# Kernel tuning notes

Hardware: AMD Instinct MI355X
Metric: run time of the kernel (lower is better)

Reference implementation:

```python
import jax, jax.numpy as jnp
import numpy as np
import math

N_ROW, N_COL, MID_DIM = 16, 16, 256
B, S, D, K, N_NEURONS = 4, 4096, 1024, 8, 64


def setup_inputs() -> dict:
    key = jax.random.key(0)
    ks = jax.random.split(key, 8)
    return {
        "x": jax.random.normal(ks[0], (B, S, D), dtype=jnp.float32),
        "neuron_idx": jax.random.randint(ks[1], (B, S, K), 0, N_NEURONS),
        "neuron_weights": jax.random.uniform(ks[2], (B, S, K), dtype=jnp.float32),
        "neuron_recipe": jax.random.normal(ks[3], (N_NEURONS, N_ROW * N_COL), dtype=jnp.float32) * 0.02,
        "row_basis": jax.random.normal(ks[4], (N_ROW, D, MID_DIM), dtype=jnp.float32) * 0.02,
        "col_basis": jax.random.normal(ks[5], (N_COL, MID_DIM, D), dtype=jnp.float32) * 0.02,
        "out_w": jax.random.normal(ks[6], (D, D), dtype=jnp.float32) * 0.02,
        "out_b": jnp.zeros((D,), dtype=jnp.float32),
        "alpha": jnp.asarray(0.1, dtype=jnp.float32),
    }


def reference(x, neuron_idx, neuron_weights, neuron_recipe, row_basis, col_basis, out_w, out_b, alpha):
    Bx, Sx, Dx = x.shape
    # --- recipe routing: gather per-token recipes, softmax, weighted sum ---
    sel = neuron_recipe[neuron_idx]                     # [B,S,k,RC]
    sel = jax.nn.softmax(sel, axis=-1)
    token_recipe = jnp.sum(sel * neuron_weights[..., None], axis=2)  # [B,S,RC]
    recipe = jax.nn.softmax(token_recipe, axis=-1).reshape(Bx, Sx, N_ROW, N_COL)
    row_w = recipe.sum(axis=-1)                         # [B,S,n_row]
    col_w = recipe.sum(axis=-2)                         # [B,S,n_col]
    # --- dynamic Q/K: sum over basis middle/last axis commutes with contraction ---
    q = jnp.einsum('bsr,rm->bsm', row_w, row_basis.sum(axis=1))  # [B,S,mid]
    kk = jnp.einsum('bsc,cm->bsm', col_w, col_basis.sum(axis=2)) # [B,S,mid]
    scores = jnp.einsum('bsm,btm->bst', q, kk) / math.sqrt(MID_DIM)  # [B,S,S]
    causal = jnp.triu(jnp.ones((Sx, Sx), dtype=bool), k=1)
    scores = jnp.where(causal, -jnp.inf, scores)
    attn = jax.nn.softmax(scores, axis=-1)
    context = jnp.einsum('bst,btd->bsd', attn, x)        # [B,S,D]
    transform = jnp.einsum('bsc,cd->bsd', col_w, col_basis.sum(axis=1))  # [B,S,D]
    out = jax.nn.gelu(context + alpha * transform, approximate=False)
    return out @ out_w.T + out_b
```

## Files before the change

### kernel.cpp

```cpp
#include <hip/hip_runtime.h>
#include <hip/hip_bf16.h>
#include <math.h>

#define BB 4
#define SS 4096
#define DDIM 1024
#define KSEL 8
#define NR 16
#define NC 16
#define MID 256
#define RC 256
#define TOK (BB*SS)

typedef __hip_bfloat16 bf16;
typedef short short8 __attribute__((ext_vector_type(8)));
typedef short short4v __attribute__((ext_vector_type(4)));
typedef float floatx4 __attribute__((ext_vector_type(4)));
typedef float floatx16 __attribute__((ext_vector_type(16)));
#define MFMA16(a,b,c) __builtin_amdgcn_mfma_f32_16x16x32_bf16(a,b,c,0,0,0)
#define MFMA32(a,b,c) __builtin_amdgcn_mfma_f32_32x32x16_bf16(a,b,c,0,0,0)

__device__ __forceinline__ float uihf(unsigned v) { union { unsigned i; float f; } t; t.i = v; return t.f; }
__device__ __forceinline__ float b2f(bf16 h) { return __bfloat162float(h); }
__device__ __forceinline__ float bs2f(short s) { return uihf(((unsigned)(unsigned short)s) << 16); }
__device__ __forceinline__ short f2bs(float f) {
    bf16 h = __float2bfloat16(f);
    return *reinterpret_cast<short*>(&h);
}
__device__ __forceinline__ float loadf(const void* p, size_t i, bool f32m) {
    return f32m ? ((const float*)p)[i] : b2f(((const bf16*)p)[i]);
}

#define WS_RB   16
#define WS_CB2  4112
#define WS_CB1  8208
#define WS_CW   24592
#define WS_BIAS 286736
#define WS_QK   287760
#define WS_WB   4482064
#define WS_XT   5006352
#define WS_LV   13394960

struct DetectArgs { const void* p[9]; int n[9]; };

__global__ void k_detect(DetectArgs A, int* __restrict__ flags) {
    int b = blockIdx.x;
    int tid = threadIdx.x;
    if (b == 9) {
        float* w = (float*)flags;
        for (int i = tid; i < 24576; i += 256) w[WS_RB + i] = 0.f;
        return;
    }
    const unsigned short* u = (const unsigned short*)A.p[b];
    int n = A.n[b]; if (n > 4096) n = 4096;
    float m = 0.f;
    for (int i = tid; i < n; i += 256) {
        unsigned v = (((unsigned)u[i]) << 16) & 0x7fffffffu;
        float f = uihf(v);
        if (f == f) m = fmaxf(m, f);
    }
    for (int o = 32; o; o >>= 1) m = fmaxf(m, __shfl_xor(m, o));
    __shared__ float red[4];
    if ((tid & 63) == 0) red[tid >> 6] = m;
    __syncthreads();
    if (tid == 0) {
        float mm = fmaxf(fmaxf(red[0], red[1]), fmaxf(red[2], red[3]));
        flags[b] = (b == 1) ? 0 : (mm > 1e4f ? 1 : 0);
    }
}

__global__ void k_rbsum(const void* __restrict__ rb, float* __restrict__ ws) {
    bool f32m = ((const int*)ws)[4] != 0;
    int r = blockIdx.x >> 3, dc = blockIdx.x & 7, m = threadIdx.x;
    size_t base = (size_t)r*DDIM*MID + (size_t)dc*128*MID + m;
    float s = 0.f;
    #pragma unroll 8
    for (int d = 0; d < 128; ++d) s += loadf(rb, base + (size_t)d*MID, f32m);
    atomicAdd(&ws[WS_RB + r*MID + m], s);
}

__global__ void k_cb2(const void* __restrict__ cb, float* __restrict__ ws) {
    bool f32m = ((const int*)ws)[5] != 0;
    int row = blockIdx.x*4 + (threadIdx.x >> 6);
    int lane = threadIdx.x & 63;
    size_t base = (size_t)row*DDIM;
    float s = 0.f;
    for (int i = lane; i < DDIM; i += 64) s += loadf(cb, base + i, f32m);
    for (int o = 32; o; o >>= 1) s += __shfl_down(s, o);
    if (lane == 0) ws[WS_CB2 + row] = s;
}

__global__ void k_cb1(const void* __restrict__ cb, float* __restrict__ ws) {
    bool f32m = ((const int*)ws)[5] != 0;
    int c = blockIdx.x >> 4;
    int d = (((blockIdx.x >> 2) & 3) << 8) + threadIdx.x;
    int m0 = (blockIdx.x & 3) * 64;
    size_t base = (size_t)c*MID*DDIM + (size_t)m0*DDIM + d;
    float s = 0.f;
    #pragma unroll 8
    for (int m = 0; m < 64; ++m) s += loadf(cb, base + (size_t)m*DDIM, f32m);
    atomicAdd(&ws[WS_CB1 + c*DDIM + d], s);
}

__global__ void k_wcvt(const void* __restrict__ w, const void* __restrict__ bias,
                       float* __restrict__ ws) {
    bool wf32 = ((const int*)ws)[6] != 0, bf32 = ((const int*)ws)[7] != 0;
    short* Wb = (short*)(ws + WS_WB);
    float* biasf = ws + WS_BIAS;
    int bx = blockIdx.x, tid = threadIdx.x;
    if (bx == 512) {
        for (int i = tid; i < DDIM; i += 256) biasf[i] = loadf(bias, i, bf32);
        return;
    }
    size_t base = (size_t)bx*2048 + tid*8;
    if (wf32) {
        const float* s = (const float*)w + base;
        float4 a = *(const float4*)s, c = *(const float4*)(s + 4);
        short8 v;
        v[0]=f2bs(a.x); v[1]=f2bs(a.y); v[2]=f2bs(a.z); v[3]=f2bs(a.w);
        v[4]=f2bs(c.x); v[5]=f2bs(c.y); v[6]=f2bs(c.z); v[7]=f2bs(c.w);
        *(short8*)(Wb + base) = v;
    } else {
        *(uint4*)(Wb + base) = *(const uint4*)((const short*)w + base);
    }
}

__global__ void k_xt(const void* __restrict__ x, float* __restrict__ ws) {
    bool xf32 = ((const int*)ws)[0] != 0;
    __shared__ short T[64][72];
    int tid = threadIdx.x;
    int s0 = blockIdx.x*64, d0 = blockIdx.y*64, b = blockIdx.z;
    int rr = tid >> 4, c4 = (tid & 15)*4;
    #pragma unroll
    for (int it = 0; it < 4; ++it) {
        int r = rr + it*16;
        size_t off = (size_t)(b*SS + s0 + r)*DDIM + d0 + c4;
        float v[4];
        if (xf32) {
            float4 a = *(const float4*)((const float*)x + off);
            v[0]=a.x; v[1]=a.y; v[2]=a.z; v[3]=a.w;
        } else {
            const short* p = (const short*)x + off;
            #pragma unroll
            for (int j = 0; j < 4; ++j) v[j] = bs2f(p[j]);
        }
        #pragma unroll
        for (int j = 0; j < 4; ++j) T[c4+j][r] = f2bs(v[j]);
    }
    __syncthreads();
    int dr = tid >> 2, sc = (tid & 3)*16;
    short8 u0 = *(const short8*)(&T[dr][sc]);
    short8 u1 = *(const short8*)(&T[dr][sc+8]);
    short* dst = (short*)(ws + WS_XT) + ((size_t)(b*DDIM + d0 + dr))*SS + s0 + sc;
    *(short8*)dst = u0;
    *(short8*)(dst + 8) = u1;
}

__global__ __launch_bounds__(256) void k_route(const int* __restrict__ nidx,
        const void* __restrict__ nw, const void* __restrict__ rmat,
        float* __restrict__ ws) {
    const bool f2 = ((const int*)ws)[2] != 0, f3 = ((const int*)ws)[3] != 0;
    const int lane = threadIdx.x & 63;
    const int tok = blockIdx.x*4 + (threadIdx.x >> 6);

    int idx8 = 0; float w8 = 0.f;
    if (lane < KSEL) {
        idx8 = nidx[tok*KSEL + lane];
        w8   = loadf(nw, tok*KSEL + lane, f2);
    }

    float acc[4] = {0.f,0.f,0.f,0.f};
    #pragma unroll 1
    for (int k = 0; k < KSEL; ++k) {
        int   id_k = __shfl(idx8, k);
        float wk   = __shfl(w8, k);
        float v[4];
        if (f3) {
            float4 t = *(const float4*)((const float*)rmat + (size_t)id_k*RC + lane*4);
            v[0]=t.x; v[1]=t.y; v[2]=t.z; v[3]=t.w;
        } else {
            short4v t = *(const short4v*)((const short*)rmat + (size_t)id_k*RC + lane*4);
            #pragma unroll
            for (int j = 0; j < 4; ++j) v[j] = bs2f(t[j]);
        }
        float m = fmaxf(fmaxf(v[0],v[1]), fmaxf(v[2],v[3]));
        #pragma unroll
        for (int o = 32; o; o >>= 1) m = fmaxf(m, __shfl_xor(m, o));
        float e[4], s = 0.f;
        #pragma unroll
        for (int j = 0; j < 4; ++j) { e[j] = __expf(v[j]-m); s += e[j]; }
        #pragma unroll
        for (int o = 32; o; o >>= 1) s += __shfl_xor(s, o);
        float r = wk / s;
        #pragma unroll
        for (int j = 0; j < 4; ++j) acc[j] += r * e[j];
    }
    {
        float m = fmaxf(fmaxf(acc[0],acc[1]), fmaxf(acc[2],acc[3]));
        #pragma unroll
        for (int o = 32; o; o >>= 1) m = fmaxf(m, __shfl_xor(m, o));
        float s = 0.f;
        #pragma unroll
        for (int j = 0; j < 4; ++j) { acc[j] = __expf(acc[j]-m); s += acc[j]; }
        #pragma unroll
        for (int o = 32; o; o >>= 1) s += __shfl_xor(s, o);
        float inv = 1.f / s;
        #pragma unroll
        for (int j = 0; j < 4; ++j) acc[j] *= inv;
    }
    float rwp = acc[0]+acc[1]+acc[2]+acc[3];
    rwp += __shfl_xor(rwp, 1); rwp += __shfl_xor(rwp, 2);
    float cw4[4] = {acc[0],acc[1],acc[2],acc[3]};
    #pragma unroll
    for (int j = 0; j < 4; ++j) {
        cw4[j] += __shfl_xor(cw4[j], 4);
        cw4[j] += __shfl_xor(cw4[j], 8);
        cw4[j] += __shfl_xor(cw4[j], 16);
        cw4[j] += __shfl_xor(cw4[j], 32);
    }
    if (lane < 4) {
        float4 t; t.x=cw4[0]; t.y=cw4[1]; t.z=cw4[2]; t.w=cw4[3];
        *(float4*)(ws + WS_CW + (size_t)tok*NC + lane*4) = t;
    }
    float rwAll[NR], cwAll[NC];
    #pragma unroll
    for (int r = 0; r < NR; ++r) rwAll[r] = __shfl(rwp, r*4);
    #pragma unroll
    for (int c = 0; c < NC; ++c) cwAll[c] = __shfl(cw4[c & 3], c >> 2);
    float qv[4] = {0.f,0.f,0.f,0.f}, kv[4] = {0.f,0.f,0.f,0.f};
    #pragma unroll
    for (int r = 0; r < NR; ++r) {
        float4 t = *(const float4*)(ws + WS_RB + r*MID + lane*4);
        qv[0] += rwAll[r]*t.x; qv[1] += rwAll[r]*t.y;
        qv[2] += rwAll[r]*t.z; qv[3] += rwAll[r]*t.w;
    }
    #pragma unroll
    for (int c = 0; c < NC; ++c) {
        float4 t = *(const float4*)(ws + WS_CB2 + c*MID + lane*4);
        kv[0] += cwAll[c]*t.x; kv[1] += cwAll[c]*t.y;
        kv[2] += cwAll[c]*t.z; kv[3] += cwAll[c]*t.w;
    }
    short* Qh  = (short*)(ws + WS_QK);
    short* KKh = Qh + (size_t)TOK*MID;
    short4v qo, ko;
    #pragma unroll
    for (int j = 0; j < 4; ++j) { qo[j] = f2bs(qv[j]*0.0625f); ko[j] = f2bs(kv[j]); }
    *(short4v*)(Qh  + (size_t)tok*MID + lane*4) = qo;
    *(short4v*)(KKh + (size_t)tok*MID + lane*4) = ko;
}

__global__ __launch_bounds__(256) void k_att(const float* __restrict__ ws,
        float* __restrict__ U, const void* __restrict__ alphap) {
    __shared__ __align__(16) short Ks[32*264];
    __shared__ __align__(16) short Ps[64*40];
    __shared__ __align__(16) short cb1T[256*40];
    __shared__ __align__(16) short cwsb[64*40];
    __shared__ float lv[64];
    const int tid = threadIdx.x;
    const int w = tid >> 6, lane = tid & 63, lq = lane & 15, quad = lane >> 4;
    const int lid = blockIdx.x + (int)gridDim.x*(blockIdx.y + (int)gridDim.y*blockIdx.z);
    const int g = lid & 15;
    const int qt = (SS/64 - 1) - (lid >> 4);
    const int q0 = qt*64, d0 = (g & 3)*256, b = g >> 2;
    const bool af32 = ((const int*)ws)[8] != 0;
    const short* Qh  = (const short*)(ws + WS_QK);
    const short* KKh = Qh + (size_t)TOK*MID;
    const short* xT  = (const short*)(ws + WS_XT);

    {
        int r = tid >> 2, c4 = (tid & 3)*4;
        const float* cwp = ws + WS_CW + (size_t)(b*SS + q0 + r)*NC + c4;
        short* dst = cwsb + r*40;
        #pragma unroll
        for (int j = 0; j < 4; ++j) dst[c4 + j] = f2bs(cwp[j]);
        #pragma unroll
        for (int j = 0; j < 4; ++j) dst[16 + c4 + j] = 0;
    }
    {
        const float* src = ws + WS_CB1 + d0 + tid;
        short* dst = cb1T + tid*40;
        #pragma unroll
        for (int c = 0; c < 16; ++c) dst[c] = f2bs(src[c*DDIM]);
        #pragma unroll
        for (int c = 16; c < 32; ++c) dst[c] = 0;
    }
    short8 qa[8];
    {
        const short* qrow = Qh + (size_t)(b*SS + q0 + w*16 + lq)*MID + quad*8;
        #pragma unroll
        for (int ks = 0; ks < 8; ++ks) qa[ks] = *(const short8*)(qrow + ks*32);
    }

    floatx4 acc[4][4];
    #pragma unroll
    for (int qi = 0; qi < 4; ++qi)
        #pragma unroll
        for (int di = 0; di < 4; ++di) acc[qi][di] = (floatx4){0.f,0.f,0.f,0.f};
    float l[4] = {0.f,0.f,0.f,0.f};

    const int ntiles = 2*qt + 2;
    const short* xb_base = xT + (size_t)(b*DDIM + d0 + w*64 + lq)*SS + quad*8;
    const int rsw = (lq >> 2) & 3;
    const short* pa_rd = Ps + lq*40 + ((quad ^ rsw) << 3);
    short* pd_base = Ps + (w*16 + quad*4)*40 + (lq & 7);

    #pragma unroll 1
    for (int it = 0; it < ntiles; ++it) {
        const int t0 = it*32;
        const short* xx = xb_base + it*32;
        short8 xf0 = *(const short8*)(xx);
        short8 xf1 = *(const short8*)(xx + (size_t)16*SS);
        short8 xf2 = *(const short8*)(xx + (size_t)32*SS);
        short8 xf3 = *(const short8*)(xx + (size_t)48*SS);
        {
            int r = tid >> 3, sg = (tid & 7)*32;
            const short* src = KKh + (size_t)(b*SS + t0 + r)*MID + sg;
            short* dst = Ks + r*264 + sg;
            #pragma unroll
            for (int j = 0; j < 4; ++j)
                *(short8*)(dst + j*8) = *(const short8*)(src + j*8);
        }
        __syncthreads();
        #pragma unroll
        for (int h = 0; h < 2; ++h) {
            floatx4 s = (floatx4){0.f,0.f,0.f,0.f};
            const short* kb = Ks + (h*16 + lq)*264 + quad*8;
            #pragma unroll
            for (int ks = 0; ks < 8; ++ks)
                s = MFMA16(qa[ks], *(const short8*)(kb + ks*32), s);
            int t = t0 + h*16 + lq;
            int qg = q0 + w*16 + quad*4;
            short* pd = pd_base + (((h*2 + (lq >> 3)) ^ quad) << 3);
            #pragma unroll
            for (int r = 0; r < 4; ++r) {
                float p = (t <= qg + r) ? __expf(s[r]) : 0.f;
                l[r] += p;
                pd[r*40] = f2bs(p);
            }
        }
        __syncthreads();
        {
            short8 pa0 = *(const short8*)(pa_rd);
            short8 pa1 = *(const short8*)(pa_rd + 16*40);
            short8 pa2 = *(const short8*)(pa_rd + 32*40);
            short8 pa3 = *(const short8*)(pa_rd + 48*40);
            acc[0][0] = MFMA16(pa0, xf0, acc[0][0]);
            acc[0][1] = MFMA16(pa0, xf1, acc[0][1]);
            acc[0][2] = MFMA16(pa0, xf2, acc[0][2]);
            acc[0][3] = MFMA16(pa0, xf3, acc[0][3]);
            acc[1][0] = MFMA16(pa1, xf0, acc[1][0]);
            acc[1][1] = MFMA16(pa1, xf1, acc[1][1]);
            acc[1][2] = MFMA16(pa1, xf2, acc[1][2]);
            acc[1][3] = MFMA16(pa1, xf3, acc[1][3]);
            acc[2][0] = MFMA16(pa2, xf0, acc[2][0]);
            acc[2][1] = MFMA16(pa2, xf1, acc[2][1]);
            acc[2][2] = MFMA16(pa2, xf2, acc[2][2]);
            acc[2][3] = MFMA16(pa2, xf3, acc[2][3]);
            acc[3][0] = MFMA16(pa3, xf0, acc[3][0]);
            acc[3][1] = MFMA16(pa3, xf1, acc[3][1]);
            acc[3][2] = MFMA16(pa3, xf2, acc[3][2]);
            acc[3][3] = MFMA16(pa3, xf3, acc[3][3]);
        }
    }

    #pragma unroll
    for (int r = 0; r < 4; ++r) {
        float v = l[r];
        v += __shfl_xor(v,1); v += __shfl_xor(v,2);
        v += __shfl_xor(v,4); v += __shfl_xor(v,8);
        if (lq == 0) lv[w*16 + quad*4 + r] = v;
    }
    __syncthreads();
    float linv[4][4];
    #pragma unroll
    for (int qi = 0; qi < 4; ++qi)
        #pragma unroll
        for (int r = 0; r < 4; ++r)
            linv[qi][r] = 1.f / lv[qi*16 + quad*4 + r];

    float alpha = af32 ? ((const float*)alphap)[0] : bs2f(((const short*)alphap)[0]);
    short8 ca[4];
    #pragma unroll
    for (int qi = 0; qi < 4; ++qi)
        ca[qi] = *(const short8*)(cwsb + (qi*16 + lq)*40 + quad*8);
    #pragma unroll
    for (int di = 0; di < 4; ++di) {
        const int nt = w*4 + di;
        const short8 cbf = *(const short8*)(cb1T + (nt*16 + lq)*40 + quad*8);
        #pragma unroll
        for (int qi = 0; qi < 4; ++qi) {
            floatx4 tr = (floatx4){0.f,0.f,0.f,0.f};
            tr = MFMA16(ca[qi], cbf, tr);
            float* Ub = U + (size_t)(b*SS + q0 + qi*16 + quad*4)*DDIM + d0 + nt*16 + lq;
            #pragma unroll
            for (int r = 0; r < 4; ++r) {
                float u = acc[qi][di][r]*linv[qi][r] + alpha*tr[r];
                float e2 = __expf(1.5957691216f*(u + 0.044715f*u*u*u));
                float th = 1.f - 2.f/(e2 + 1.f);
                Ub[(size_t)r*DDIM] = 0.5f*u*(1.f + th);
            }
        }
    }
}

__global__ __launch_bounds__(256,2) void k_gemm3(float* __restrict__ out,
        const float* __restrict__ ws) {
    __shared__ __align__(16) short Al[32*132];
    const int tid = threadIdx.x;
    const int w = tid >> 6, lane = tid & 63;
    const int col = lane & 31, kh = lane >> 5;
    const int m0 = blockIdx.x*32;
    const int n0 = w*256;
    const short* Wb = (const short*)(ws + WS_WB);
    const float* biasf = ws + WS_BIAS;

    floatx16 acc[8];
    #pragma unroll
    for (int nt = 0; nt < 8; ++nt)
        #pragma unroll
        for (int r = 0; r < 16; ++r) acc[nt][r] = 0.f;

    const int srow = tid >> 3, sk = (tid & 7)*16;
    const float* Usrc = out + (size_t)(m0 + srow)*DDIM + sk;
    short* Adst = Al + srow*132 + sk;

    #pragma unroll 1
    for (int kc = 0; kc < DDIM; kc += 128) {
        __syncthreads();
        {
            const float* s = Usrc + kc;
            float4 a = *(const float4*)s,     b4 = *(const float4*)(s + 4);
            float4 c = *(const float4*)(s+8), d  = *(const float4*)(s + 12);
            short8 v0, v1;
            v0[0]=f2bs(a.x);  v0[1]=f2bs(a.y);  v0[2]=f2bs(a.z);  v0[3]=f2bs(a.w);
            v0[4]=f2bs(b4.x); v0[5]=f2bs(b4.y); v0[6]=f2bs(b4.z); v0[7]=f2bs(b4.w);
            v1[0]=f2bs(c.x);  v1[1]=f2bs(c.y);  v1[2]=f2bs(c.z);  v1[3]=f2bs(c.w);
            v1[4]=f2bs(d.x);  v1[5]=f2bs(d.y);  v1[6]=f2bs(d.z);  v1[7]=f2bs(d.w);
            *(short8*)(Adst)     = v0;
            *(short8*)(Adst + 8) = v1;
        }
        __syncthreads();
        const short* wbp0 = Wb + (size_t)(n0 + col)*DDIM + kc + kh*8;
        #pragma unroll
        for (int ks = 0; ks < 8; ++ks) {
            short8 af = *(const short8*)(Al + col*132 + ks*16 + kh*8);
            const short* wbp = wbp0 + ks*16;
            #pragma unroll
            for (int nt = 0; nt < 8; ++nt)
                acc[nt] = MFMA32(af, *(const short8*)(wbp + (size_t)nt*32*DDIM), acc[nt]);
        }
    }
    #pragma unroll
    for (int nt = 0; nt < 8; ++nt) {
        int c = n0 + nt*32 + col;
        float bb = biasf[c];
        #pragma unroll
        for (int r = 0; r < 16; ++r) {
            int row = (r & 3) + 8*(r >> 2) + 4*kh;
            out[(size_t)(m0 + row)*DDIM + c] = acc[nt][r] + bb;
        }
    }
}

extern "C" void kernel_launch(void* const* d_in, const int* in_sizes, int n_in,
                              void* d_out, int out_size, void* d_ws, size_t ws_size,
                              hipStream_t stream) {
    (void)out_size; (void)ws_size;
    const void* x    = d_in[0];
    const int*  nidx = (const int*)d_in[1];
    const void* nw   = d_in[2];
    const void* rmat = d_in[3];
    const void* rb   = d_in[4];
    const void* cb   = d_in[5];
    const void* w    = d_in[6];
    const void* bias = d_in[7];
    const void* alpha= d_in[8];
    float* ws = (float*)d_ws;
    float* out = (float*)d_out;

    DetectArgs da;
    for (int i = 0; i < 9; ++i) { da.p[i] = d_in[i]; da.n[i] = (i < n_in) ? in_sizes[i] : 1; }

    k_detect<<<10, 256, 0, stream>>>(da, (int*)ws);
    k_rbsum<<<128, 256, 0, stream>>>(rb, ws);
    k_cb2  <<<1024, 256, 0, stream>>>(cb, ws);
    k_cb1  <<<256, 256, 0, stream>>>(cb, ws);
    k_wcvt <<<513, 256, 0, stream>>>(w, bias, ws);
    k_xt   <<<dim3(SS/64, DDIM/64, BB), 256, 0, stream>>>(x, ws);
    k_route<<<TOK/4, 256, 0, stream>>>(nidx, nw, rmat, ws);
    k_att  <<<dim3(SS/64, DDIM/256, BB), 256, 0, stream>>>(ws, out, alpha);
    k_gemm3<<<TOK/32, 256, 0, stream>>>(out, ws);
}
```

Measured before the change: 626.3 us.

## Widen attention D-tile to 512, pair causal q-tiles per block, prefetch K

The attention kernel now covers 512 output columns per block instead of 256, which halves how often the QK^T scores and exp are recomputed across D-splits. Each block handles two query tiles (qt and 63-qt), so causal work is balanced evenly and the grid is 256 blocks. K rows for the next tile are prefetched into registers before the LDS store. The trade-off is twice the accumulator registers and a larger LDS footprint, which may lower occupancy, and fewer blocks in flight.

```diff
diff --git a/kernel.cpp b/kernel.cpp
--- a/kernel.cpp
+++ b/kernel.cpp
@@ -253,151 +253,186 @@
         float* __restrict__ U, const void* __restrict__ alphap) {
     __shared__ __align__(16) short Ks[32*264];
     __shared__ __align__(16) short Ps[64*40];
-    __shared__ __align__(16) short cb1T[256*40];
+    __shared__ __align__(16) short cb1T[512*40];
     __shared__ __align__(16) short cwsb[64*40];
     __shared__ float lv[64];
     const int tid = threadIdx.x;
     const int w = tid >> 6, lane = tid & 63, lq = lane & 15, quad = lane >> 4;
-    const int lid = blockIdx.x + (int)gridDim.x*(blockIdx.y + (int)gridDim.y*blockIdx.z);
-    const int g = lid & 15;
-    const int qt = (SS/64 - 1) - (lid >> 4);
-    const int q0 = qt*64, d0 = (g & 3)*256, b = g >> 2;
+    const int d0 = blockIdx.x*512, b = blockIdx.y, qtp = blockIdx.z;
     const bool af32 = ((const int*)ws)[8] != 0;
     const short* Qh  = (const short*)(ws + WS_QK);
     const short* KKh = Qh + (size_t)TOK*MID;
     const short* xT  = (const short*)(ws + WS_XT);
 
     {
-        int r = tid >> 2, c4 = (tid & 3)*4;
-        const float* cwp = ws + WS_CW + (size_t)(b*SS + q0 + r)*NC + c4;
-        short* dst = cwsb + r*40;
-        #pragma unroll
-        for (int j = 0; j < 4; ++j) dst[c4 + j] = f2bs(cwp[j]);
-        #pragma unroll
-        for (int j = 0; j < 4; ++j) dst[16 + c4 + j] = 0;
-    }
-    {
-        const float* src = ws + WS_CB1 + d0 + tid;
-        short* dst = cb1T + tid*40;
-        #pragma unroll
-        for (int c = 0; c < 16; ++c) dst[c] = f2bs(src[c*DDIM]);
-        #pragma unroll
-        for (int c = 16; c < 32; ++c) dst[c] = 0;
-    }
-    short8 qa[8];
-    {
-        const short* qrow = Qh + (size_t)(b*SS + q0 + w*16 + lq)*MID + quad*8;
-        #pragma unroll
-        for (int ks = 0; ks < 8; ++ks) qa[ks] = *(const short8*)(qrow + ks*32);
-    }
-
-    floatx4 acc[4][4];
-    #pragma unroll
-    for (int qi = 0; qi < 4; ++qi)
-        #pragma unroll
-        for (int di = 0; di < 4; ++di) acc[qi][di] = (floatx4){0.f,0.f,0.f,0.f};
-    float l[4] = {0.f,0.f,0.f,0.f};
-
-    const int ntiles = 2*qt + 2;
-    const short* xb_base = xT + (size_t)(b*DDIM + d0 + w*64 + lq)*SS + quad*8;
+        for (int r = tid; r < 512; r += 256) {
+            const float* src = ws + WS_CB1 + d0 + r;
+            short* dst = cb1T + r*40;
+            #pragma unroll
+            for (int c = 0; c < 16; ++c) dst[c] = f2bs(src[c*DDIM]);
+            #pragma unroll
+            for (int c = 16; c < 32; ++c) dst[c] = 0;
+        }
+    }
     const int rsw = (lq >> 2) & 3;
     const short* pa_rd = Ps + lq*40 + ((quad ^ rsw) << 3);
     short* pd_base = Ps + (w*16 + quad*4)*40 + (lq & 7);
+    const int kr = tid >> 3, ksg = (tid & 7)*32;
+    short* kdst = Ks + kr*264 + ksg;
+    float alpha = af32 ? ((const float*)alphap)[0] : bs2f(((const short*)alphap)[0]);
 
     #pragma unroll 1
-    for (int it = 0; it < ntiles; ++it) {
-        const int t0 = it*32;
-        const short* xx = xb_base + it*32;
-        short8 xf0 = *(const short8*)(xx);
-        short8 xf1 = *(const short8*)(xx + (size_t)16*SS);
-        short8 xf2 = *(const short8*)(xx + (size_t)32*SS);
-        short8 xf3 = *(const short8*)(xx + (size_t)48*SS);
-        {
-            int r = tid >> 3, sg = (tid & 7)*32;
-            const short* src = KKh + (size_t)(b*SS + t0 + r)*MID + sg;
-            short* dst = Ks + r*264 + sg;
-            #pragma unroll
-            for (int j = 0; j < 4; ++j)
-                *(short8*)(dst + j*8) = *(const short8*)(src + j*8);
-        }
-        __syncthreads();
-        #pragma unroll
-        for (int h = 0; h < 2; ++h) {
-            floatx4 s = (floatx4){0.f,0.f,0.f,0.f};
-            const short* kb = Ks + (h*16 + lq)*264 + quad*8;
-            #pragma unroll
-            for (int ks = 0; ks < 8; ++ks)
-                s = MFMA16(qa[ks], *(const short8*)(kb + ks*32), s);
-            int t = t0 + h*16 + lq;
-            int qg = q0 + w*16 + quad*4;
-            short* pd = pd_base + (((h*2 + (lq >> 3)) ^ quad) << 3);
-            #pragma unroll
-            for (int r = 0; r < 4; ++r) {
-                float p = (t <= qg + r) ? __expf(s[r]) : 0.f;
-                l[r] += p;
-                pd[r*40] = f2bs(p);
-            }
-        }
+    for (int ph = 0; ph < 2; ++ph) {
+        const int qt = ph ? qtp : 63 - qtp;
+        const int q0 = qt*64;
+        const int ntiles = 2*qt + 2;
         __syncthreads();
         {
-            short8 pa0 = *(const short8*)(pa_rd);
-            short8 pa1 = *(const short8*)(pa_rd + 16*40);
-            short8 pa2 = *(const short8*)(pa_rd + 32*40);
-            short8 pa3 = *(const short8*)(pa_rd + 48*40);
-            acc[0][0] = MFMA16(pa0, xf0, acc[0][0]);
-            acc[0][1] = MFMA16(pa0, xf1, acc[0][1]);
-            acc[0][2] = MFMA16(pa0, xf2, acc[0][2]);
-            acc[0][3] = MFMA16(pa0, xf3, acc[0][3]);
-            acc[1][0] = MFMA16(pa1, xf0, acc[1][0]);
-            acc[1][1] = MFMA16(pa1, xf1, acc[1][1]);
-            acc[1][2] = MFMA16(pa1, xf2, acc[1][2]);
-            acc[1][3] = MFMA16(pa1, xf3, acc[1][3]);
-            acc[2][0] = MFMA16(pa2, xf0, acc[2][0]);
-            acc[2][1] = MFMA16(pa2, xf1, acc[2][1]);
-            acc[2][2] = MFMA16(pa2, xf2, acc[2][2]);
-            acc[2][3] = MFMA16(pa2, xf3, acc[2][3]);
-            acc[3][0] = MFMA16(pa3, xf0, acc[3][0]);
-            acc[3][1] = MFMA16(pa3, xf1, acc[3][1]);
-            acc[3][2] = MFMA16(pa3, xf2, acc[3][2]);
-            acc[3][3] = MFMA16(pa3, xf3, acc[3][3]);
-        }
-    }
-
-    #pragma unroll
-    for (int r = 0; r < 4; ++r) {
-        float v = l[r];
-        v += __shfl_xor(v,1); v += __shfl_xor(v,2);
-        v += __shfl_xor(v,4); v += __shfl_xor(v,8);
-        if (lq == 0) lv[w*16 + quad*4 + r] = v;
-    }
-    __syncthreads();
-    float linv[4][4];
-    #pragma unroll
-    for (int qi = 0; qi < 4; ++qi)
-        #pragma unroll
-        for (int r = 0; r < 4; ++r)
-            linv[qi][r] = 1.f / lv[qi*16 + quad*4 + r];
-
-    float alpha = af32 ? ((const float*)alphap)[0] : bs2f(((const short*)alphap)[0]);
-    short8 ca[4];
-    #pragma unroll
-    for (int qi = 0; qi < 4; ++qi)
-        ca[qi] = *(const short8*)(cwsb + (qi*16 + lq)*40 + quad*8);
-    #pragma unroll
-    for (int di = 0; di < 4; ++di) {
-        const int nt = w*4 + di;
-        const short8 cbf = *(const short8*)(cb1T + (nt*16 + lq)*40 + quad*8);
-        #pragma unroll
-        for (int qi = 0; qi < 4; ++qi) {
-            floatx4 tr = (floatx4){0.f,0.f,0.f,0.f};
-            tr = MFMA16(ca[qi], cbf, tr);
-            float* Ub = U + (size_t)(b*SS + q0 + qi*16 + quad*4)*DDIM + d0 + nt*16 + lq;
-            #pragma unroll
-            for (int r = 0; r < 4; ++r) {
-                float u = acc[qi][di][r]*linv[qi][r] + alpha*tr[r];
-                float e2 = __expf(1.5957691216f*(u + 0.044715f*u*u*u));
-                float th = 1.f - 2.f/(e2 + 1.f);
-                Ub[(size_t)r*DDIM] = 0.5f*u*(1.f + th);
+            int r = tid >> 2, c4 = (tid & 3)*4;
+            const float* cwp = ws + WS_CW + (size_t)(b*SS + q0 + r)*NC + c4;
+            short* dst = cwsb + r*40;
+            #pragma unroll
+            for (int j = 0; j < 4; ++j) dst[c4 + j] = f2bs(cwp[j]);
+            #pragma unroll
+            for (int j = 0; j < 4; ++j) dst[16 + c4 + j] = 0;
+        }
+        short8 qa[8];
+        {
+            const short* qrow = Qh + (size_t)(b*SS + q0 + w*16 + lq)*MID + quad*8;
+            #pragma unroll
+            for (int ks = 0; ks < 8; ++ks) qa[ks] = *(const short8*)(qrow + ks*32);
+        }
+        floatx4 acc[4][8];
+        #pragma unroll
+        for (int qi = 0; qi < 4; ++qi)
+            #pragma unroll
+            for (int di = 0; di < 8; ++di) acc[qi][di] = (floatx4){0.f,0.f,0.f,0.f};
+        float l[4] = {0.f,0.f,0.f,0.f};
+
+        const short* xb_base = xT + (size_t)(b*DDIM + d0 + w*128 + lq)*SS + quad*8;
+        const short* ksrc0 = KKh + (size_t)(b*SS + kr)*MID + ksg;
+        short8 kp0 = *(const short8*)(ksrc0);
+        short8 kp1 = *(const short8*)(ksrc0 + 8);
+        short8 kp2 = *(const short8*)(ksrc0 + 16);
+        short8 kp3 = *(const short8*)(ksrc0 + 24);
+
+        #pragma unroll 1
+        for (int it = 0; it < ntiles; ++it) {
+            const int t0 = it*32;
+            *(short8*)(kdst)      = kp0;
+            *(short8*)(kdst + 8)  = kp1;
+            *(short8*)(kdst + 16) = kp2;
+            *(short8*)(kdst + 24) = kp3;
+            if (it + 1 < ntiles) {
+                const short* ks_n = ksrc0 + (size_t)(it + 1)*32*MID;
+                kp0 = *(const short8*)(ks_n);
+                kp1 = *(const short8*)(ks_n + 8);
+                kp2 = *(const short8*)(ks_n + 16);
+                kp3 = *(const short8*)(ks_n + 24);
+            }
+            const short* xx = xb_base + it*32;
+            short8 xf0 = *(const short8*)(xx);
+            short8 xf1 = *(const short8*)(xx + (size_t)16*SS);
+            short8 xf2 = *(const short8*)(xx + (size_t)32*SS);
+            short8 xf3 = *(const short8*)(xx + (size_t)48*SS);
+            short8 xf4 = *(const short8*)(xx + (size_t)64*SS);
+            short8 xf5 = *(const short8*)(xx + (size_t)80*SS);
+            short8 xf6 = *(const short8*)(xx + (size_t)96*SS);
+            short8 xf7 = *(const short8*)(xx + (size_t)112*SS);
+            __syncthreads();
+            #pragma unroll
+            for (int h = 0; h < 2; ++h) {
+                floatx4 s = (floatx4){0.f,0.f,0.f,0.f};
+                const short* kb = Ks + (h*16 + lq)*264 + quad*8;
+                #pragma unroll
+                for (int ks = 0; ks < 8; ++ks)
+                    s = MFMA16(qa[ks], *(const short8*)(kb + ks*32), s);
+                int t = t0 + h*16 + lq;
+                int qg = q0 + w*16 + quad*4;
+                short* pd = pd_base + (((h*2 + (lq >> 3)) ^ quad) << 3);
+                #pragma unroll
+                for (int r = 0; r < 4; ++r) {
+                    float p = (t <= qg + r) ? __expf(s[r]) : 0.f;
+                    l[r] += p;
+                    pd[r*40] = f2bs(p);
+                }
+            }
+            __syncthreads();
+            {
+                short8 pa0 = *(const short8*)(pa_rd);
+                short8 pa1 = *(const short8*)(pa_rd + 16*40);
+                short8 pa2 = *(const short8*)(pa_rd + 32*40);
+                short8 pa3 = *(const short8*)(pa_rd + 48*40);
+                acc[0][0] = MFMA16(pa0, xf0, acc[0][0]);
+                acc[1][0] = MFMA16(pa1, xf0, acc[1][0]);
+                acc[2][0] = MFMA16(pa2, xf0, acc[2][0]);
+                acc[3][0] = MFMA16(pa3, xf0, acc[3][0]);
+                acc[0][1] = MFMA16(pa0, xf1, acc[0][1]);
+                acc[1][1] = MFMA16(pa1, xf1, acc[1][1]);
+                acc[2][1] = MFMA16(pa2, xf1, acc[2][1]);
+                acc[3][1] = MFMA16(pa3, xf1, acc[3][1]);
+                acc[0][2] = MFMA16(pa0, xf2, acc[0][2]);
+                acc[1][2] = MFMA16(pa1, xf2, acc[1][2]);
+                acc[2][2] = MFMA16(pa2, xf2, acc[2][2]);
+                acc[3][2] = MFMA16(pa3, xf2, acc[3][2]);
+                acc[0][3] = MFMA16(pa0, xf3, acc[0][3]);
+                acc[1][3] = MFMA16(pa1, xf3, acc[1][3]);
+                acc[2][3] = MFMA16(pa2, xf3, acc[2][3]);
+                acc[3][3] = MFMA16(pa3, xf3, acc[3][3]);
+                acc[0][4] = MFMA16(pa0, xf4, acc[0][4]);
+                acc[1][4] = MFMA16(pa1, xf4, acc[1][4]);
+                acc[2][4] = MFMA16(pa2, xf4, acc[2][4]);
+                acc[3][4] = MFMA16(pa3, xf4, acc[3][4]);
+                acc[0][5] = MFMA16(pa0, xf5, acc[0][5]);
+                acc[1][5] = MFMA16(pa1, xf5, acc[1][5]);
+                acc[2][5] = MFMA16(pa2, xf5, acc[2][5]);
+                acc[3][5] = MFMA16(pa3, xf5, acc[3][5]);
+                acc[0][6] = MFMA16(pa0, xf6, acc[0][6]);
+                acc[1][6] = MFMA16(pa1, xf6, acc[1][6]);
+                acc[2][6] = MFMA16(pa2, xf6, acc[2][6]);
+                acc[3][6] = MFMA16(pa3, xf6, acc[3][6]);
+                acc[0][7] = MFMA16(pa0, xf7, acc[0][7]);
+                acc[1][7] = MFMA16(pa1, xf7, acc[1][7]);
+                acc[2][7] = MFMA16(pa2, xf7, acc[2][7]);
+                acc[3][7] = MFMA16(pa3, xf7, acc[3][7]);
+            }
+        }
+
+        #pragma unroll
+        for (int r = 0; r < 4; ++r) {
+            float v = l[r];
+            v += __shfl_xor(v,1); v += __shfl_xor(v,2);
+            v += __shfl_xor(v,4); v += __shfl_xor(v,8);
+            if (lq == 0) lv[w*16 + quad*4 + r] = v;
+        }
+        __syncthreads();
+        float linv[4][4];
+        #pragma unroll
+        for (int qi = 0; qi < 4; ++qi)
+            #pragma unroll
+            for (int r = 0; r < 4; ++r)
+                linv[qi][r] = 1.f / lv[qi*16 + quad*4 + r];
+
+        short8 ca[4];
+        #pragma unroll
+        for (int qi = 0; qi < 4; ++qi)
+            ca[qi] = *(const short8*)(cwsb + (qi*16 + lq)*40 + quad*8);
+        #pragma unroll
+        for (int di = 0; di < 8; ++di) {
+            const int dl = w*128 + di*16;
+            const short8 cbf = *(const short8*)(cb1T + (dl + lq)*40 + quad*8);
+            #pragma unroll
+            for (int qi = 0; qi < 4; ++qi) {
+                floatx4 tr = (floatx4){0.f,0.f,0.f,0.f};
+                tr = MFMA16(ca[qi], cbf, tr);
+                float* Ub = U + (size_t)(b*SS + q0 + qi*16 + quad*4)*DDIM + d0 + dl + lq;
+                #pragma unroll
+                for (int r = 0; r < 4; ++r) {
+                    float u = acc[qi][di][r]*linv[qi][r] + alpha*tr[r];
+                    float e2 = __expf(1.5957691216f*(u + 0.044715f*u*u*u));
+                    float th = 1.f - 2.f/(e2 + 1.f);
+                    Ub[(size_t)r*DDIM] = 0.5f*u*(1.f + th);
+                }
             }
         }
     }
@@ -488,6 +523,6 @@
     k_wcvt <<<513, 256, 0, stream>>>(w, bias, ws);
     k_xt   <<<dim3(SS/64, DDIM/64, BB), 256, 0, stream>>>(x, ws);
     k_route<<<TOK/4, 256, 0, stream>>>(nidx, nw, rmat, ws);
-    k_att  <<<dim3(SS/64, DDIM/256, BB), 256, 0, stream>>>(ws, out, alpha);
+    k_att  <<<dim3(2, BB, 32), 256, 0, stream>>>(ws, out, alpha);
     k_gemm3<<<TOK/32, 256, 0, stream>>>(out, ws);
 }
```

Measured after the change: 612.5 us. 2.2% less time.

## Warp-specialize attention kernel into QK producers and PV consumers with paired causal tiles

Applied to the files above, without the earlier changes.

Reworks the attention kernel into 512-thread blocks in which four waves compute QK scores and exponentials into a double-buffered P tile while four other waves run the PV MFMAs and the GELU epilogue, so the two phases overlap. Each block now covers 512 output columns instead of 256, halving QK recomputation across column blocks. Each block processes a short and a long causal query tile (qt and 63-qt) to balance work, and K rows are prefetched into registers. In exchange there are more barriers per tile, higher register pressure from 32 accumulators per consumer wave, and fewer blocks in the grid (256 instead of 1024).

```diff
diff --git a/kernel.cpp b/kernel.cpp
--- a/kernel.cpp
+++ b/kernel.cpp
@@ -249,34 +249,24 @@
     *(short4v*)(KKh + (size_t)tok*MID + lane*4) = ko;
 }
 
-__global__ __launch_bounds__(256) void k_att(const float* __restrict__ ws,
+__global__ __launch_bounds__(512) void k_att(const float* __restrict__ ws,
         float* __restrict__ U, const void* __restrict__ alphap) {
     __shared__ __align__(16) short Ks[32*264];
-    __shared__ __align__(16) short Ps[64*40];
-    __shared__ __align__(16) short cb1T[256*40];
+    __shared__ __align__(16) short Ps[2*64*40];
+    __shared__ __align__(16) short cb1T[512*40];
     __shared__ __align__(16) short cwsb[64*40];
     __shared__ float lv[64];
     const int tid = threadIdx.x;
     const int w = tid >> 6, lane = tid & 63, lq = lane & 15, quad = lane >> 4;
-    const int lid = blockIdx.x + (int)gridDim.x*(blockIdx.y + (int)gridDim.y*blockIdx.z);
-    const int g = lid & 15;
-    const int qt = (SS/64 - 1) - (lid >> 4);
-    const int q0 = qt*64, d0 = (g & 3)*256, b = g >> 2;
+    const bool prod = (w < 4);
+    const int wp = w & 3;
+    const int d0 = blockIdx.x*512, b = blockIdx.y, qtp = blockIdx.z;
     const bool af32 = ((const int*)ws)[8] != 0;
     const short* Qh  = (const short*)(ws + WS_QK);
     const short* KKh = Qh + (size_t)TOK*MID;
     const short* xT  = (const short*)(ws + WS_XT);
 
     {
-        int r = tid >> 2, c4 = (tid & 3)*4;
-        const float* cwp = ws + WS_CW + (size_t)(b*SS + q0 + r)*NC + c4;
-        short* dst = cwsb + r*40;
-        #pragma unroll
-        for (int j = 0; j < 4; ++j) dst[c4 + j] = f2bs(cwp[j]);
-        #pragma unroll
-        for (int j = 0; j < 4; ++j) dst[16 + c4 + j] = 0;
-    }
-    {
         const float* src = ws + WS_CB1 + d0 + tid;
         short* dst = cb1T + tid*40;
         #pragma unroll
@@ -284,123 +274,203 @@
         #pragma unroll
         for (int c = 16; c < 32; ++c) dst[c] = 0;
     }
-    short8 qa[8];
-    {
-        const short* qrow = Qh + (size_t)(b*SS + q0 + w*16 + lq)*MID + quad*8;
-        #pragma unroll
-        for (int ks = 0; ks < 8; ++ks) qa[ks] = *(const short8*)(qrow + ks*32);
-    }
-
-    floatx4 acc[4][4];
-    #pragma unroll
-    for (int qi = 0; qi < 4; ++qi)
-        #pragma unroll
-        for (int di = 0; di < 4; ++di) acc[qi][di] = (floatx4){0.f,0.f,0.f,0.f};
-    float l[4] = {0.f,0.f,0.f,0.f};
-
-    const int ntiles = 2*qt + 2;
-    const short* xb_base = xT + (size_t)(b*DDIM + d0 + w*64 + lq)*SS + quad*8;
+
     const int rsw = (lq >> 2) & 3;
     const short* pa_rd = Ps + lq*40 + ((quad ^ rsw) << 3);
-    short* pd_base = Ps + (w*16 + quad*4)*40 + (lq & 7);
+    short* pd_base = Ps + (wp*16 + quad*4)*40 + (lq & 7);
+    const int kr = tid >> 3, ksg = (tid & 7)*32;
+    short* kdst = Ks + kr*264 + ksg;
+    const short* ksrc0 = KKh + (size_t)(b*SS + kr)*MID + ksg;
+    const short* xb_base = xT + (size_t)(b*DDIM + d0 + wp*128 + lq)*SS + quad*8;
+    float alpha = af32 ? ((const float*)alphap)[0] : bs2f(((const short*)alphap)[0]);
+
+    short8 qa[8];
+    short8 kp0, kp1, kp2, kp3;
+    floatx4 acc[4][8];
+    short8 xs0, xs1, xs2, xs3, xs4, xs5, xs6, xs7;
+    float l[4];
+
+#define KSTAGE() do { \
+    *(short8*)(kdst)      = kp0; \
+    *(short8*)(kdst + 8)  = kp1; \
+    *(short8*)(kdst + 16) = kp2; \
+    *(short8*)(kdst + 24) = kp3; \
+} while (0)
+#define KPREF(IT) do { \
+    const short* kn_ = ksrc0 + (size_t)(IT)*32*MID; \
+    kp0 = *(const short8*)(kn_); \
+    kp1 = *(const short8*)(kn_ + 8); \
+    kp2 = *(const short8*)(kn_ + 16); \
+    kp3 = *(const short8*)(kn_ + 24); \
+} while (0)
+#define QK(IT, PSOFF) do { \
+    const int t0_ = (IT)*32; \
+    _Pragma("unroll") \
+    for (int h = 0; h < 2; ++h) { \
+        floatx4 s_ = (floatx4){0.f,0.f,0.f,0.f}; \
+        const short* kb_ = Ks + (h*16 + lq)*264 + quad*8; \
+        _Pragma("unroll") \
+        for (int ks = 0; ks < 8; ++ks) \
+            s_ = MFMA16(qa[ks], *(const short8*)(kb_ + ks*32), s_); \
+        int t_ = t0_ + h*16 + lq; \
+        short* pd_ = pd_base + (PSOFF) + (((h*2 + (lq >> 3)) ^ quad) << 3); \
+        _Pragma("unroll") \
+        for (int r = 0; r < 4; ++r) { \
+            float p_ = (t_ <= qg + r) ? __expf(s_[r]) : 0.f; \
+            l[r] += p_; \
+            pd_[r*40] = f2bs(p_); \
+        } \
+    } \
+} while (0)
+#define PVS(PSOFF) do { \
+    const short* pr_ = pa_rd + (PSOFF); \
+    short8 pa0 = *(const short8*)(pr_); \
+    short8 pa1 = *(const short8*)(pr_ + 640); \
+    short8 pa2 = *(const short8*)(pr_ + 1280); \
+    short8 pa3 = *(const short8*)(pr_ + 1920); \
+    acc[0][0] = MFMA16(pa0, xs0, acc[0][0]); \
+    acc[1][0] = MFMA16(pa1, xs0, acc[1][0]); \
+    acc[2][0] = MFMA16(pa2, xs0, acc[2][0]); \
+    acc[3][0] = MFMA16(pa3, xs0, acc[3][0]); \
+    acc[0][1] = MFMA16(pa0, xs1, acc[0][1]); \
+    acc[1][1] = MFMA16(pa1, xs1, acc[1][1]); \
+    acc[2][1] = MFMA16(pa2, xs1, acc[2][1]); \
+    acc[3][1] = MFMA16(pa3, xs1, acc[3][1]); \
+    acc[0][2] = MFMA16(pa0, xs2, acc[0][2]); \
+    acc[1][2] = MFMA16(pa1, xs2, acc[1][2]); \
+    acc[2][2] = MFMA16(pa2, xs2, acc[2][2]); \
+    acc[3][2] = MFMA16(pa3, xs2, acc[3][2]); \
+    acc[0][3] = MFMA16(pa0, xs3, acc[0][3]); \
+    acc[1][3] = MFMA16(pa1, xs3, acc[1][3]); \
+    acc[2][3] = MFMA16(pa2, xs3, acc[2][3]); \
+    acc[3][3] = MFMA16(pa3, xs3, acc[3][3]); \
+    acc[0][4] = MFMA16(pa0, xs4, acc[0][4]); \
+    acc[1][4] = MFMA16(pa1, xs4, acc[1][4]); \
+    acc[2][4] = MFMA16(pa2, xs4, acc[2][4]); \
+    acc[3][4] = MFMA16(pa3, xs4, acc[3][4]); \
+    acc[0][5] = MFMA16(pa0, xs5, acc[0][5]); \
+    acc[1][5] = MFMA16(pa1, xs5, acc[1][5]); \
+    acc[2][5] = MFMA16(pa2, xs5, acc[2][5]); \
+    acc[3][5] = MFMA16(pa3, xs5, acc[3][5]); \
+    acc[0][6] = MFMA16(pa0, xs6, acc[0][6]); \
+    acc[1][6] = MFMA16(pa1, xs6, acc[1][6]); \
+    acc[2][6] = MFMA16(pa2, xs6, acc[2][6]); \
+    acc[3][6] = MFMA16(pa3, xs6, acc[3][6]); \
+    acc[0][7] = MFMA16(pa0, xs7, acc[0][7]); \
+    acc[1][7] = MFMA16(pa1, xs7, acc[1][7]); \
+    acc[2][7] = MFMA16(pa2, xs7, acc[2][7]); \
+    acc[3][7] = MFMA16(pa3, xs7, acc[3][7]); \
+} while (0)
+#define XLOAD(IT) do { \
+    const short* xx_ = xb_base + (IT)*32; \
+    xs0 = *(const short8*)(xx_); \
+    xs1 = *(const short8*)(xx_ + (size_t)16*SS); \
+    xs2 = *(const short8*)(xx_ + (size_t)32*SS); \
+    xs3 = *(const short8*)(xx_ + (size_t)48*SS); \
+    xs4 = *(const short8*)(xx_ + (size_t)64*SS); \
+    xs5 = *(const short8*)(xx_ + (size_t)80*SS); \
+    xs6 = *(const short8*)(xx_ + (size_t)96*SS); \
+    xs7 = *(const short8*)(xx_ + (size_t)112*SS); \
+} while (0)
 
     #pragma unroll 1
-    for (int it = 0; it < ntiles; ++it) {
-        const int t0 = it*32;
-        const short* xx = xb_base + it*32;
-        short8 xf0 = *(const short8*)(xx);
-        short8 xf1 = *(const short8*)(xx + (size_t)16*SS);
-        short8 xf2 = *(const short8*)(xx + (size_t)32*SS);
-        short8 xf3 = *(const short8*)(xx + (size_t)48*SS);
-        {
-            int r = tid >> 3, sg = (tid & 7)*32;
-            const short* src = KKh + (size_t)(b*SS + t0 + r)*MID + sg;
-            short* dst = Ks + r*264 + sg;
-            #pragma unroll
-            for (int j = 0; j < 4; ++j)
-                *(short8*)(dst + j*8) = *(const short8*)(src + j*8);
-        }
+    for (int ph = 0; ph < 2; ++ph) {
+        const int qt = ph ? qtp : 63 - qtp;
+        const int q0 = qt*64;
+        const int ntiles = 2*qt + 2;
+        const int qg = q0 + wp*16 + quad*4;
         __syncthreads();
-        #pragma unroll
-        for (int h = 0; h < 2; ++h) {
-            floatx4 s = (floatx4){0.f,0.f,0.f,0.f};
-            const short* kb = Ks + (h*16 + lq)*264 + quad*8;
-            #pragma unroll
-            for (int ks = 0; ks < 8; ++ks)
-                s = MFMA16(qa[ks], *(const short8*)(kb + ks*32), s);
-            int t = t0 + h*16 + lq;
-            int qg = q0 + w*16 + quad*4;
-            short* pd = pd_base + (((h*2 + (lq >> 3)) ^ quad) << 3);
+        if (tid < 256) {
+            int r = tid >> 2, c4 = (tid & 3)*4;
+            const float* cwp = ws + WS_CW + (size_t)(b*SS + q0 + r)*NC + c4;
+            short* dst = cwsb + r*40;
+            #pragma unroll
+            for (int j = 0; j < 4; ++j) dst[c4 + j] = f2bs(cwp[j]);
+            #pragma unroll
+            for (int j = 0; j < 4; ++j) dst[16 + c4 + j] = 0;
+        }
+        if (prod) {
+            const short* qrow = Qh + (size_t)(b*SS + q0 + wp*16 + lq)*MID + quad*8;
+            #pragma unroll
+            for (int ks = 0; ks < 8; ++ks) qa[ks] = *(const short8*)(qrow + ks*32);
+            KPREF(0);
+            l[0] = l[1] = l[2] = l[3] = 0.f;
+        } else {
+            #pragma unroll
+            for (int qi = 0; qi < 4; ++qi)
+                #pragma unroll
+                for (int di = 0; di < 8; ++di) acc[qi][di] = (floatx4){0.f,0.f,0.f,0.f};
+        }
+
+        #pragma unroll 1
+        for (int it = 0; it < ntiles; it += 2) {
+            if (prod) { KSTAGE(); KPREF(it + 1); }
+            __syncthreads();
+            if (prod) {
+                QK(it, 0);
+            } else {
+                if (it > 0) PVS(2560);
+                XLOAD(it);
+            }
+            __syncthreads();
+            if (prod) { KSTAGE(); if (it + 2 < ntiles) KPREF(it + 2); }
+            __syncthreads();
+            if (prod) {
+                QK(it + 1, 2560);
+            } else {
+                PVS(0);
+                XLOAD(it + 1);
+            }
+            __syncthreads();
+        }
+        if (prod) {
             #pragma unroll
             for (int r = 0; r < 4; ++r) {
-                float p = (t <= qg + r) ? __expf(s[r]) : 0.f;
-                l[r] += p;
-                pd[r*40] = f2bs(p);
+                float v = l[r];
+                v += __shfl_xor(v,1); v += __shfl_xor(v,2);
+                v += __shfl_xor(v,4); v += __shfl_xor(v,8);
+                if (lq == 0) lv[wp*16 + quad*4 + r] = v;
             }
+        } else {
+            PVS(2560);
         }
         __syncthreads();
-        {
-            short8 pa0 = *(const short8*)(pa_rd);
-            short8 pa1 = *(const short8*)(pa_rd + 16*40);
-            short8 pa2 = *(const short8*)(pa_rd + 32*40);
-            short8 pa3 = *(const short8*)(pa_rd + 48*40);
-            acc[0][0] = MFMA16(pa0, xf0, acc[0][0]);
-            acc[0][1] = MFMA16(pa0, xf1, acc[0][1]);
-            acc[0][2] = MFMA16(pa0, xf2, acc[0][2]);
-            acc[0][3] = MFMA16(pa0, xf3, acc[0][3]);
-            acc[1][0] = MFMA16(pa1, xf0, acc[1][0]);
-            acc[1][1] = MFMA16(pa1, xf1, acc[1][1]);
-            acc[1][2] = MFMA16(pa1, xf2, acc[1][2]);
-            acc[1][3] = MFMA16(pa1, xf3, acc[1][3]);
-            acc[2][0] = MFMA16(pa2, xf0, acc[2][0]);
-            acc[2][1] = MFMA16(pa2, xf1, acc[2][1]);
-            acc[2][2] = MFMA16(pa2, xf2, acc[2][2]);
-            acc[2][3] = MFMA16(pa2, xf3, acc[2][3]);
-            acc[3][0] = MFMA16(pa3, xf0, acc[3][0]);
-            acc[3][1] = MFMA16(pa3, xf1, acc[3][1]);
-            acc[3][2] = MFMA16(pa3, xf2, acc[3][2]);
-            acc[3][3] = MFMA16(pa3, xf3, acc[3][3]);
-        }
-    }
-
-    #pragma unroll
-    for (int r = 0; r < 4; ++r) {
-        float v = l[r];
-        v += __shfl_xor(v,1); v += __shfl_xor(v,2);
-        v += __shfl_xor(v,4); v += __shfl_xor(v,8);
-        if (lq == 0) lv[w*16 + quad*4 + r] = v;
-    }
-    __syncthreads();
-    float linv[4][4];
-    #pragma unroll
-    for (int qi = 0; qi < 4; ++qi)
-        #pragma unroll
-        for (int r = 0; r < 4; ++r)
-            linv[qi][r] = 1.f / lv[qi*16 + quad*4 + r];
-
-    float alpha = af32 ? ((const float*)alphap)[0] : bs2f(((const short*)alphap)[0]);
-    short8 ca[4];
-    #pragma unroll
-    for (int qi = 0; qi < 4; ++qi)
-        ca[qi] = *(const short8*)(cwsb + (qi*16 + lq)*40 + quad*8);
-    #pragma unroll
-    for (int di = 0; di < 4; ++di) {
-        const int nt = w*4 + di;
-        const short8 cbf = *(const short8*)(cb1T + (nt*16 + lq)*40 + quad*8);
-        #pragma unroll
-        for (int qi = 0; qi < 4; ++qi) {
-            floatx4 tr = (floatx4){0.f,0.f,0.f,0.f};
-            tr = MFMA16(ca[qi], cbf, tr);
-            float* Ub = U + (size_t)(b*SS + q0 + qi*16 + quad*4)*DDIM + d0 + nt*16 + lq;
-            #pragma unroll
-            for (int r = 0; r < 4; ++r) {
-                float u = acc[qi][di][r]*linv[qi][r] + alpha*tr[r];
-                float e2 = __expf(1.5957691216f*(u + 0.044715f*u*u*u));
-                float th = 1.f - 2.f/(e2 + 1.f);
-                Ub[(size_t)r*DDIM] = 0.5f*u*(1.f + th);
+        if (!prod) {
+            float linv[4][4];
+            #pragma unroll
+            for (int qi = 0; qi < 4; ++qi)
+                #pragma unroll
+                for (int r = 0; r < 4; ++r)
+                    linv[qi][r] = 1.f / lv[qi*16 + quad*4 + r];
+            short8 ca[4];
+            #pragma unroll
+            for (int qi = 0; qi < 4; ++qi)
+                ca[qi] = *(const short8*)(cwsb + (qi*16 + lq)*40 + quad*8);
+            #pragma unroll
+            for (int di = 0; di < 8; ++di) {
+                const int dl = wp*128 + di*16;
+                const short8 cbf = *(const short8*)(cb1T + (dl + lq)*40 + quad*8);
+                #pragma unroll
+                for (int qi = 0; qi < 4; ++qi) {
+                    floatx4 tr = (floatx4){0.f,0.f,0.f,0.f};
+                    tr = MFMA16(ca[qi], cbf, tr);
+                    float* Ub = U + (size_t)(b*SS + q0 + qi*16 + quad*4)*DDIM + d0 + dl + lq;
+                    #pragma unroll
+                    for (int r = 0; r < 4; ++r) {
+                        float u = acc[qi][di][r]*linv[qi][r] + alpha*tr[r];
+                        float e2 = __expf(1.5957691216f*(u + 0.044715f*u*u*u));
+                        float th = 1.f - 2.f/(e2 + 1.f);
+                        Ub[(size_t)r*DDIM] = 0.5f*u*(1.f + th);
+                    }
+                }
             }
         }
     }
+#undef KSTAGE
+#undef KPREF
+#undef QK
+#undef PVS
+#undef XLOAD
 }
 
 __global__ __launch_bounds__(256,2) void k_gemm3(float* __restrict__ out,
@@ -488,6 +558,6 @@
     k_wcvt <<<513, 256, 0, stream>>>(w, bias, ws);
     k_xt   <<<dim3(SS/64, DDIM/64, BB), 256, 0, stream>>>(x, ws);
     k_route<<<TOK/4, 256, 0, stream>>>(nidx, nw, rmat, ws);
-    k_att  <<<dim3(SS/64, DDIM/256, BB), 256, 0, stream>>>(ws, out, alpha);
+    k_att  <<<dim3(2, BB, 32), 512, 0, stream>>>(ws, out, alpha);
     k_gemm3<<<TOK/32, 256, 0, stream>>>(out, ws);
 }
```

Measured after the change: 631.7 us. No clear change (+0.9%).
